# Optimization experiments

Measured on AMD Instinct MI355X. Metric: run time of the kernel, lower is better.

## Reference

```python
import jax, jax.numpy as jnp
import numpy as np

N = 100000
E = 1600000
IN_F, HID, OUT_F = 256, 128, 64


def setup_inputs() -> dict:
    key = jax.random.key(0)
    k_x, k_e, k_w1, k_w2, k_b1, k_b2 = jax.random.split(key, 6)
    x = jax.random.normal(k_x, (N, IN_F), dtype=jnp.float32)
    edge_index = jax.random.randint(k_e, (2, E), 0, N, dtype=jnp.int32)
    # GCNConv params: lin has no bias in PyG; separate additive bias per layer.
    W1 = jax.random.normal(k_w1, (IN_F, HID), dtype=jnp.float32) / np.sqrt(IN_F)
    b1 = jax.random.normal(k_b1, (HID,), dtype=jnp.float32) * 0.01
    W2 = jax.random.normal(k_w2, (HID, OUT_F), dtype=jnp.float32) / np.sqrt(HID)
    b2 = jax.random.normal(k_b2, (OUT_F,), dtype=jnp.float32) * 0.01
    return {"x": x, "edge_index": edge_index, "W1": W1, "b1": b1, "W2": W2, "b2": b2}


def _gcn_norm(edge_index, num_nodes):
    # add self loops (improved=False -> weight 1.0), symmetric normalization
    loop = jnp.arange(num_nodes, dtype=edge_index.dtype)
    src = jnp.concatenate([edge_index[0], loop])
    dst = jnp.concatenate([edge_index[1], loop])
    w = jnp.ones(src.shape[0], dtype=jnp.float32)
    deg = jax.ops.segment_sum(w, dst, num_segments=num_nodes)
    dinv = jnp.where(deg > 0, jax.lax.rsqrt(deg), 0.0)
    norm = dinv[src] * w * dinv[dst]
    return src, dst, norm


def _gcn_layer(h, W, b, src, dst, norm, num_nodes):
    h = h @ W                               # [N, out]
    msg = h[src] * norm[:, None]            # [E+N, out] gather + scale
    out = jax.ops.segment_sum(msg, dst, num_segments=num_nodes)  # scatter-add
    return out + b


def reference(x, edge_index, W1, b1, W2, b2):
    # dropout is identity in eval mode
    src, dst, norm = _gcn_norm(edge_index, N)
    h = _gcn_layer(x, W1, b1, src, dst, norm, N)
    h = jax.nn.relu(h)
    out = _gcn_layer(h, W2, b2, src, dst, norm, N)
    return out
```

## Files before the change

kernel.cpp:

```cpp
#include <hip/hip_runtime.h>
#include <hip/hip_bf16.h>

#define N_NODES 100000
#define N_EDGES 1600000
#define IN_FEAT 256
#define HID_F   128
#define OUT_FT  64

#define NBUK   256
#define NPB    391
#define BUKCAP 8192
#define EPB    4096
#define G_BIN  ((N_EDGES + EPB - 1) / EPB)
#define G_GEMM ((N_NODES + 63) / 64)
#define G_CAST ((IN_FEAT * HID_F + HID_F * OUT_FT + 255) / 256)
#define G_AGG  ((N_NODES + 7) / 8)

typedef unsigned short u16;
typedef __attribute__((ext_vector_type(8))) unsigned short u16x8;
typedef __attribute__((ext_vector_type(8))) short short8;
typedef __attribute__((ext_vector_type(4))) float f32x4;

static __device__ inline u16 f2bf(float f) {
    __hip_bfloat16 h = __float2bfloat16(f);
    return *reinterpret_cast<u16*>(&h);
}
static __device__ inline float bf2f(u16 u) {
    union { unsigned u; float f; } c;
    c.u = ((unsigned)u) << 16;
    return c.f;
}


__global__ __launch_bounds__(256) void k_bin(const int* __restrict__ srcA,
                                             const int* __restrict__ dstA,
                                             int* __restrict__ gcur, int2* __restrict__ pairs,
                                             const float* __restrict__ W1,
                                             const float* __restrict__ W2,
                                             u16* __restrict__ W1t, u16* __restrict__ W2t) {
    if (blockIdx.x >= G_BIN) {
        int idx = (blockIdx.x - G_BIN) * 256 + threadIdx.x;
        if (idx < IN_FEAT * HID_F) {
            int k = idx / HID_F, n = idx % HID_F;
            W1t[n * IN_FEAT + k] = f2bf(W1[idx]);
        } else {
            int e2 = idx - IN_FEAT * HID_F;
            if (e2 < HID_F * OUT_FT) {
                int k = e2 / OUT_FT, n = e2 % OUT_FT;
                W2t[n * HID_F + k] = f2bf(W2[e2]);
            }
        }
        return;
    }
    __shared__ int lh[NBUK];
    int t = threadIdx.x;
    int e0 = blockIdx.x * EPB;
    if (t < NBUK) lh[t] = 0;
    __syncthreads();
#pragma unroll
    for (int i = 0; i < EPB / 256; i++) {
        int e = e0 + i * 256 + t;
        if (e < N_EDGES) atomicAdd(&lh[dstA[e] / NPB], 1);
    }
    __syncthreads();
    if (t < NBUK) {
        int c = lh[t];
        lh[t] = atomicAdd(&gcur[t], c);
    }
    __syncthreads();
#pragma unroll
    for (int i = 0; i < EPB / 256; i++) {
        int e = e0 + i * 256 + t;
        if (e < N_EDGES) {
            int d = dstA[e];
            int b = d / NPB;
            int p = atomicAdd(&lh[b], 1);
            if (p < BUKCAP) pairs[(size_t)b * BUKCAP + p] = make_int2(srcA[e], d);
        }
    }
}


__global__ __launch_bounds__(256) void k_fillB(const int2* __restrict__ pairs,
                                               const int* __restrict__ gcnt,
                                               int* __restrict__ offsets,
                                               float* __restrict__ dinv,
                                               int* __restrict__ csr) {
    __shared__ int hist[NPB];
    __shared__ int sm[256];
    __shared__ int s_ebase;
    int b = blockIdx.x, t = threadIdx.x;
    int nbase = b * NPB;
    int nn = min(NPB, N_NODES - nbase);

    int gv = gcnt[t];
    sm[t] = gv;
    __syncthreads();
    for (int o = 1; o < 256; o <<= 1) {
        int u = (t >= o) ? sm[t - o] : 0;
        __syncthreads();
        sm[t] += u;
        __syncthreads();
    }
    if (t == b) s_ebase = sm[t] - gv;
    __syncthreads();
    int ebase = s_ebase;
    int cnt = gcnt[b];
    const int2* pb = pairs + (size_t)b * BUKCAP;

    for (int i = t; i < NPB; i += 256) hist[i] = 0;
    __syncthreads();
    for (int i = t; i < cnt; i += 256) atomicAdd(&hist[pb[i].y - nbase], 1);
    __syncthreads();

    int base2 = t * 2;
    int c0 = (base2 < NPB) ? hist[base2] : 0;
    int c1 = (base2 + 1 < NPB) ? hist[base2 + 1] : 0;
    int s = c0 + c1;
    __syncthreads();
    sm[t] = s;
    __syncthreads();
    for (int o = 1; o < 256; o <<= 1) {
        int u = (t >= o) ? sm[t - o] : 0;
        __syncthreads();
        sm[t] += u;
        __syncthreads();
    }
    int run = ebase + sm[t] - s;
    __syncthreads();
    int cc[2] = {c0, c1};
#pragma unroll
    for (int q = 0; q < 2; q++) {
        int n = base2 + q;
        if (n < nn) {
            int g = nbase + n;
            offsets[g] = run;
            dinv[g] = rsqrtf((float)(cc[q] + 1));
            hist[n] = run;
            run += cc[q];
        }
    }
    __syncthreads();
    for (int i = t; i < cnt; i += 256) {
        int2 e = pb[i];
        int p = atomicAdd(&hist[e.y - nbase], 1);
        csr[p] = e.x;
    }
    if (b == NBUK - 1 && t == 0) offsets[N_NODES] = N_EDGES;
}


__global__ __launch_bounds__(256) void k_gemm1(const float* __restrict__ A,
                                               const u16* __restrict__ Bt,
                                               const float* __restrict__ dinv,
                                               u16* __restrict__ C) {
    int tid = threadIdx.x;
    int wv = tid >> 6, lane = tid & 63;
    int m16 = lane & 15, quad = lane >> 4;
    int rowbase = blockIdx.x * 64 + wv * 16;
    int row_a = rowbase + m16;
    if (row_a >= N_NODES) row_a = N_NODES - 1;

    f32x4 acc[8];
#pragma unroll
    for (int j = 0; j < 8; j++) acc[j] = (f32x4)(0.f);

    const float* arow = &A[(size_t)row_a * IN_FEAT + quad * 8];

#pragma unroll 2
    for (int k0 = 0; k0 < IN_FEAT; k0 += 32) {
        f32x4 a0 = *(const f32x4*)&arow[k0];
        f32x4 a1 = *(const f32x4*)&arow[k0 + 4];
        u16x8 af;
#pragma unroll
        for (int j = 0; j < 4; j++) { af[j] = f2bf(a0[j]); af[4 + j] = f2bf(a1[j]); }
        short8 afs = *(short8*)&af;
#pragma unroll
        for (int ct = 0; ct < 8; ct++) {
            short8 bf = *(const short8*)&Bt[(size_t)(16 * ct + m16) * IN_FEAT + k0 + quad * 8];
            acc[ct] = __builtin_amdgcn_mfma_f32_16x16x32_bf16(afs, bf, acc[ct], 0, 0, 0);
        }
    }

#pragma unroll
    for (int r4 = 0; r4 < 4; r4++) {
        int grow = rowbase + quad * 4 + r4;
        if (grow < N_NODES) {
            float dv = dinv[grow];
#pragma unroll
            for (int ct = 0; ct < 8; ct++)
                C[(size_t)grow * HID_F + 16 * ct + m16] = f2bf(acc[ct][r4] * dv);
        }
    }
}


__global__ __launch_bounds__(256) void k_gemm2(const u16* __restrict__ A,
                                               const u16* __restrict__ Bt,
                                               const float* __restrict__ dinv,
                                               u16* __restrict__ C) {
    int tid = threadIdx.x;
    int wv = tid >> 6, lane = tid & 63;
    int m16 = lane & 15, quad = lane >> 4;
    int rowbase = blockIdx.x * 64 + wv * 16;
    int row_a = rowbase + m16;
    if (row_a >= N_NODES) row_a = N_NODES - 1;

    f32x4 acc[4];
#pragma unroll
    for (int j = 0; j < 4; j++) acc[j] = (f32x4)(0.f);

    const u16* arow = &A[(size_t)row_a * HID_F + quad * 8];

#pragma unroll
    for (int k0 = 0; k0 < HID_F; k0 += 32) {
        short8 afs = *(const short8*)&arow[k0];
#pragma unroll
        for (int ct = 0; ct < 4; ct++) {
            short8 bf = *(const short8*)&Bt[(size_t)(16 * ct + m16) * HID_F + k0 + quad * 8];
            acc[ct] = __builtin_amdgcn_mfma_f32_16x16x32_bf16(afs, bf, acc[ct], 0, 0, 0);
        }
    }

#pragma unroll
    for (int r4 = 0; r4 < 4; r4++) {
        int grow = rowbase + quad * 4 + r4;
        if (grow < N_NODES) {
            float dv = dinv[grow];
#pragma unroll
            for (int ct = 0; ct < 4; ct++)
                C[(size_t)grow * OUT_FT + 16 * ct + m16] = f2bf(acc[ct][r4] * dv);
        }
    }
}


__global__ __launch_bounds__(256) void k_agg1(const u16* __restrict__ hs,
                                              const int* __restrict__ offsets,
                                              const int* __restrict__ csr,
                                              const float* __restrict__ dinv,
                                              const float* __restrict__ b,
                                              u16* __restrict__ out) {
    int wave = threadIdx.x >> 6;
    int lane = threadIdx.x & 63;
    int half = lane >> 5;
    int node = blockIdx.x * 8 + wave * 2 + half;
    if (node >= N_NODES) return;
    int gl = lane & 31;
    int g = gl >> 4;
    int fl = gl & 15;
    const int fo = fl * 8;
    int beg = offsets[node], end = offsets[node + 1];

    float accA[8], accB[8];
#pragma unroll
    for (int i = 0; i < 8; i++) { accA[i] = 0.f; accB[i] = 0.f; }

    int j = beg;
    for (; j + 8 <= end; j += 8) {
        int s0 = csr[j + g];
        int s1 = csr[j + 2 + g];
        int s2 = csr[j + 4 + g];
        int s3 = csr[j + 6 + g];
        u16x8 r0 = *(const u16x8*)&hs[(size_t)s0 * HID_F + fo];
        u16x8 r1 = *(const u16x8*)&hs[(size_t)s1 * HID_F + fo];
        u16x8 r2 = *(const u16x8*)&hs[(size_t)s2 * HID_F + fo];
        u16x8 r3 = *(const u16x8*)&hs[(size_t)s3 * HID_F + fo];
#pragma unroll
        for (int i = 0; i < 8; i++) {
            accA[i] += bf2f(r0[i]) + bf2f(r1[i]);
            accB[i] += bf2f(r2[i]) + bf2f(r3[i]);
        }
    }
    if (j + 4 <= end) {
        int s0 = csr[j + g];
        int s1 = csr[j + 2 + g];
        u16x8 r0 = *(const u16x8*)&hs[(size_t)s0 * HID_F + fo];
        u16x8 r1 = *(const u16x8*)&hs[(size_t)s1 * HID_F + fo];
#pragma unroll
        for (int i = 0; i < 8; i++) accA[i] += bf2f(r0[i]) + bf2f(r1[i]);
        j += 4;
    }
    for (; j < end; j += 2) {
        int idx = j + g;
        if (idx < end) {
            int s = csr[idx];
            u16x8 r0 = *(const u16x8*)&hs[(size_t)s * HID_F + fo];
#pragma unroll
            for (int i = 0; i < 8; i++) accB[i] += bf2f(r0[i]);
        }
    }
#pragma unroll
    for (int i = 0; i < 8; i++) {
        float v = accA[i] + accB[i];
        v += __shfl_xor(v, 16, 64);
        accA[i] = v;
    }
    if (g == 0) {
        u16x8 sr = *(const u16x8*)&hs[(size_t)node * HID_F + fo];
        float dv = dinv[node];
        f32x4 b0 = *(const f32x4*)&b[fo];
        f32x4 b1 = *(const f32x4*)&b[fo + 4];
        u16x8 o;
#pragma unroll
        for (int i = 0; i < 4; i++) {
            o[i]     = f2bf(fmaxf(dv * (accA[i]     + bf2f(sr[i]))     + b0[i], 0.f));
            o[4 + i] = f2bf(fmaxf(dv * (accA[4 + i] + bf2f(sr[4 + i])) + b1[i], 0.f));
        }
        *(u16x8*)&out[(size_t)node * HID_F + fo] = o;
    }
}


__global__ __launch_bounds__(256) void k_agg2(const u16* __restrict__ hs,
                                              const int* __restrict__ offsets,
                                              const int* __restrict__ csr,
                                              const float* __restrict__ dinv,
                                              const float* __restrict__ b,
                                              float* __restrict__ out) {
    int wave = threadIdx.x >> 6;
    int lane = threadIdx.x & 63;
    int half = lane >> 5;
    int node = blockIdx.x * 8 + wave * 2 + half;
    if (node >= N_NODES) return;
    int gl = lane & 31;
    int g = gl >> 3;
    int fl = gl & 7;
    const int fo = fl * 8;
    int beg = offsets[node], end = offsets[node + 1];

    float accA[8], accB[8];
#pragma unroll
    for (int i = 0; i < 8; i++) { accA[i] = 0.f; accB[i] = 0.f; }

    int j = beg;
    for (; j + 16 <= end; j += 16) {
        int s0 = csr[j + g];
        int s1 = csr[j + 4 + g];
        int s2 = csr[j + 8 + g];
        int s3 = csr[j + 12 + g];
        u16x8 r0 = *(const u16x8*)&hs[(size_t)s0 * OUT_FT + fo];
        u16x8 r1 = *(const u16x8*)&hs[(size_t)s1 * OUT_FT + fo];
        u16x8 r2 = *(const u16x8*)&hs[(size_t)s2 * OUT_FT + fo];
        u16x8 r3 = *(const u16x8*)&hs[(size_t)s3 * OUT_FT + fo];
#pragma unroll
        for (int i = 0; i < 8; i++) {
            accA[i] += bf2f(r0[i]) + bf2f(r1[i]);
            accB[i] += bf2f(r2[i]) + bf2f(r3[i]);
        }
    }
    if (j + 8 <= end) {
        int s0 = csr[j + g];
        int s1 = csr[j + 4 + g];
        u16x8 r0 = *(const u16x8*)&hs[(size_t)s0 * OUT_FT + fo];
        u16x8 r1 = *(const u16x8*)&hs[(size_t)s1 * OUT_FT + fo];
#pragma unroll
        for (int i = 0; i < 8; i++) accA[i] += bf2f(r0[i]) + bf2f(r1[i]);
        j += 8;
    }
    for (; j < end; j += 4) {
        int idx = j + g;
        if (idx < end) {
            int s = csr[idx];
            u16x8 r0 = *(const u16x8*)&hs[(size_t)s * OUT_FT + fo];
#pragma unroll
            for (int i = 0; i < 8; i++) accB[i] += bf2f(r0[i]);
        }
    }
#pragma unroll
    for (int i = 0; i < 8; i++) {
        float v = accA[i] + accB[i];
        v += __shfl_xor(v, 8, 64);
        v += __shfl_xor(v, 16, 64);
        accA[i] = v;
    }
    if (g == 0) {
        u16x8 sr = *(const u16x8*)&hs[(size_t)node * OUT_FT + fo];
        float dv = dinv[node];
        f32x4 b0 = *(const f32x4*)&b[fo];
        f32x4 b1 = *(const f32x4*)&b[fo + 4];
        f32x4 o0, o1;
#pragma unroll
        for (int i = 0; i < 4; i++) {
            o0[i] = dv * (accA[i]     + bf2f(sr[i]))     + b0[i];
            o1[i] = dv * (accA[4 + i] + bf2f(sr[4 + i])) + b1[i];
        }
        *(f32x4*)&out[(size_t)node * OUT_FT + fo] = o0;
        *(f32x4*)&out[(size_t)node * OUT_FT + fo + 4] = o1;
    }
}


extern "C" void kernel_launch(void* const* d_in, const int* in_sizes, int n_in,
                              void* d_out, int out_size, void* d_ws, size_t ws_size,
                              hipStream_t stream) {
    const float* x  = (const float*)d_in[0];
    const int*   ei = (const int*)d_in[1];
    const float* W1 = (const float*)d_in[2];
    const float* b1 = (const float*)d_in[3];
    const float* W2 = (const float*)d_in[4];
    const float* b2 = (const float*)d_in[5];
    float* out = (float*)d_out;

    char* ws = (char*)d_ws;
    int*   offsets = (int*)(ws + 0);
    float* dinv    = (float*)(ws + 400512);
    int*   csr     = (int*)(ws + 800512);
    u16*   W1t     = (u16*)(ws + 7200512);
    u16*   W2t     = (u16*)(ws + 7266048);
    int*   gcur    = (int*)(ws + 7282432);
    u16*   hs1     = (u16*)(ws + 7284608);
    u16*   a1      = (u16*)(ws + 32884608);
    int2*  pairs   = (int2*)(ws + 32884608);
    u16*   hs2     = hs1;

    const int* srcA = ei;
    const int* dstA = ei + N_EDGES;

    hipMemsetAsync(gcur, 0, NBUK * sizeof(int), stream);

    k_bin<<<G_BIN + G_CAST, 256, 0, stream>>>(srcA, dstA, gcur, pairs, W1, W2, W1t, W2t);
    k_fillB<<<NBUK, 256, 0, stream>>>(pairs, gcur, offsets, dinv, csr);

    k_gemm1<<<G_GEMM, 256, 0, stream>>>(x, W1t, dinv, hs1);
    k_agg1<<<G_AGG, 256, 0, stream>>>(hs1, offsets, csr, dinv, b1, a1);
    k_gemm2<<<G_GEMM, 256, 0, stream>>>(a1, W2t, dinv, hs2);
    k_agg2<<<G_AGG, 256, 0, stream>>>(hs2, offsets, csr, dinv, b2, out);
}
```

Before: 382.6 us.

## Stage GEMM tiles in double-buffered shared memory with register prefetch

Both node-feature GEMM kernels now load A and B K-slices cooperatively into padded, double-buffered LDS tiles. The next slice is prefetched into registers while MFMAs run on the current buffer. Before this, each wave read its B fragments directly from global memory, so the weight matrix was fetched four times per block. The change adds LDS traffic and one barrier per K-step, and these GEMMs are a small share of a pipeline dominated by gather and scatter.

```diff
diff --git a/kernel.cpp b/kernel.cpp
--- a/kernel.cpp
+++ b/kernel.cpp
@@ -154,37 +154,68 @@
                                                const u16* __restrict__ Bt,
                                                const float* __restrict__ dinv,
                                                u16* __restrict__ C) {
+    __shared__ u16 As[2][64][40];
+    __shared__ u16 Bs[2][128][40];
     int tid = threadIdx.x;
     int wv = tid >> 6, lane = tid & 63;
     int m16 = lane & 15, quad = lane >> 4;
-    int rowbase = blockIdx.x * 64 + wv * 16;
-    int row_a = rowbase + m16;
-    if (row_a >= N_NODES) row_a = N_NODES - 1;
+    int row0 = blockIdx.x * 64;
+
+    int ar = tid >> 2, aq = tid & 3;
+    int br = tid >> 1, bh = tid & 1;
+    int arow_g = row0 + ar;
+    if (arow_g >= N_NODES) arow_g = N_NODES - 1;
+    const float* ap = &A[(size_t)arow_g * IN_FEAT + aq * 8];
+    const u16*   bp = &Bt[(size_t)br * IN_FEAT + bh * 16];
 
     f32x4 acc[8];
 #pragma unroll
     for (int j = 0; j < 8; j++) acc[j] = (f32x4)(0.f);
 
-    const float* arow = &A[(size_t)row_a * IN_FEAT + quad * 8];
-
-#pragma unroll 2
-    for (int k0 = 0; k0 < IN_FEAT; k0 += 32) {
-        f32x4 a0 = *(const f32x4*)&arow[k0];
-        f32x4 a1 = *(const f32x4*)&arow[k0 + 4];
-        u16x8 af;
-#pragma unroll
-        for (int j = 0; j < 4; j++) { af[j] = f2bf(a0[j]); af[4 + j] = f2bf(a1[j]); }
-        short8 afs = *(short8*)&af;
+    {
+        f32x4 a0 = *(const f32x4*)&ap[0];
+        f32x4 a1 = *(const f32x4*)&ap[4];
+        u16x8 b0 = *(const u16x8*)&bp[0];
+        u16x8 b1 = *(const u16x8*)&bp[8];
+        u16x8 av;
+#pragma unroll
+        for (int j = 0; j < 4; j++) { av[j] = f2bf(a0[j]); av[4 + j] = f2bf(a1[j]); }
+        *(u16x8*)&As[0][ar][aq * 8] = av;
+        *(u16x8*)&Bs[0][br][bh * 16] = b0;
+        *(u16x8*)&Bs[0][br][bh * 16 + 8] = b1;
+    }
+
+#pragma unroll
+    for (int s = 0; s < 8; s++) {
+        const int buf = s & 1;
+        f32x4 na0, na1; u16x8 nb0, nb1;
+        if (s + 1 < 8) {
+            int k0 = (s + 1) * 32;
+            na0 = *(const f32x4*)&ap[k0];
+            na1 = *(const f32x4*)&ap[k0 + 4];
+            nb0 = *(const u16x8*)&bp[k0];
+            nb1 = *(const u16x8*)&bp[k0 + 8];
+        }
+        __syncthreads();
+        short8 af = *(const short8*)&As[buf][wv * 16 + m16][quad * 8];
 #pragma unroll
         for (int ct = 0; ct < 8; ct++) {
-            short8 bf = *(const short8*)&Bt[(size_t)(16 * ct + m16) * IN_FEAT + k0 + quad * 8];
-            acc[ct] = __builtin_amdgcn_mfma_f32_16x16x32_bf16(afs, bf, acc[ct], 0, 0, 0);
+            short8 bf = *(const short8*)&Bs[buf][16 * ct + m16][quad * 8];
+            acc[ct] = __builtin_amdgcn_mfma_f32_16x16x32_bf16(af, bf, acc[ct], 0, 0, 0);
+        }
+        if (s + 1 < 8) {
+            u16x8 av;
+#pragma unroll
+            for (int j = 0; j < 4; j++) { av[j] = f2bf(na0[j]); av[4 + j] = f2bf(na1[j]); }
+            *(u16x8*)&As[buf ^ 1][ar][aq * 8] = av;
+            *(u16x8*)&Bs[buf ^ 1][br][bh * 16] = nb0;
+            *(u16x8*)&Bs[buf ^ 1][br][bh * 16 + 8] = nb1;
         }
     }
 
 #pragma unroll
     for (int r4 = 0; r4 < 4; r4++) {
-        int grow = rowbase + quad * 4 + r4;
+        int grow = row0 + wv * 16 + quad * 4 + r4;
         if (grow < N_NODES) {
             float dv = dinv[grow];
 #pragma unroll
@@ -199,32 +230,55 @@
                                                const u16* __restrict__ Bt,
                                                const float* __restrict__ dinv,
                                                u16* __restrict__ C) {
+    __shared__ u16 As[2][64][40];
+    __shared__ u16 Bs[2][64][40];
     int tid = threadIdx.x;
     int wv = tid >> 6, lane = tid & 63;
     int m16 = lane & 15, quad = lane >> 4;
-    int rowbase = blockIdx.x * 64 + wv * 16;
-    int row_a = rowbase + m16;
-    if (row_a >= N_NODES) row_a = N_NODES - 1;
+    int row0 = blockIdx.x * 64;
+
+    int ar = tid >> 2, aq = tid & 3;
+    int arow_g = row0 + ar;
+    if (arow_g >= N_NODES) arow_g = N_NODES - 1;
+    const u16* ap = &A[(size_t)arow_g * HID_F + aq * 8];
+    const u16* bp = &Bt[(size_t)ar * HID_F + aq * 8];
 
     f32x4 acc[4];
 #pragma unroll
     for (int j = 0; j < 4; j++) acc[j] = (f32x4)(0.f);
 
-    const u16* arow = &A[(size_t)row_a * HID_F + quad * 8];
-
-#pragma unroll
-    for (int k0 = 0; k0 < HID_F; k0 += 32) {
-        short8 afs = *(const short8*)&arow[k0];
+    {
+        u16x8 a0 = *(const u16x8*)&ap[0];
+        u16x8 b0 = *(const u16x8*)&bp[0];
+        *(u16x8*)&As[0][ar][aq * 8] = a0;
+        *(u16x8*)&Bs[0][ar][aq * 8] = b0;
+    }
+
+#pragma unroll
+    for (int s = 0; s < 4; s++) {
+        const int buf = s & 1;
+        u16x8 na, nb;
+        if (s + 1 < 4) {
+            int k0 = (s + 1) * 32;
+            na = *(const u16x8*)&ap[k0];
+            nb = *(const u16x8*)&bp[k0];
+        }
+        __syncthreads();
+        short8 af = *(const short8*)&As[buf][wv * 16 + m16][quad * 8];
 #pragma unroll
         for (int ct = 0; ct < 4; ct++) {
-            short8 bf = *(const short8*)&Bt[(size_t)(16 * ct + m16) * HID_F + k0 + quad * 8];
-            acc[ct] = __builtin_amdgcn_mfma_f32_16x16x32_bf16(afs, bf, acc[ct], 0, 0, 0);
+            short8 bf = *(const short8*)&Bs[buf][16 * ct + m16][quad * 8];
+            acc[ct] = __builtin_amdgcn_mfma_f32_16x16x32_bf16(af, bf, acc[ct], 0, 0, 0);
+        }
+        if (s + 1 < 4) {
+            *(u16x8*)&As[buf ^ 1][ar][aq * 8] = na;
+            *(u16x8*)&Bs[buf ^ 1][ar][aq * 8] = nb;
         }
     }
 
 #pragma unroll
     for (int r4 = 0; r4 < 4; r4++) {
-        int grow = rowbase + quad * 4 + r4;
+        int grow = row0 + wv * 16 + quad * 4 + r4;
         if (grow < N_NODES) {
             float dv = dinv[grow];
 #pragma unroll
```

Result: faster. 338.2 us (-11.6%).
